# Optimization experiments

Measured on AMD Instinct MI355X. Metric: run time of the kernel, lower is better.

Reference implementation:

```python
import jax, jax.numpy as jnp
import numpy as np

B, C, L, H = 4, 512, 2048, 8
D = C // H  # head_dim


def setup_inputs() -> dict:
    key = jax.random.key(0)
    ks = jax.random.split(key, 9)
    s = 1.0 / np.sqrt(C)  # keep logits well-scaled like torch Linear init
    return {
        "x": jax.random.normal(ks[0], (B, C, L), dtype=jnp.float32),
        "Wq": jax.random.normal(ks[1], (C, C), dtype=jnp.float32) * s,
        "bq": jnp.zeros((C,), dtype=jnp.float32),
        "Wk": jax.random.normal(ks[2], (C, C), dtype=jnp.float32) * s,
        "bk": jnp.zeros((C,), dtype=jnp.float32),
        "Wv": jax.random.normal(ks[3], (C, C), dtype=jnp.float32) * s,
        "bv": jnp.zeros((C,), dtype=jnp.float32),
        "Wo": jax.random.normal(ks[4], (C, C), dtype=jnp.float32) * s,
        "bo": jnp.zeros((C,), dtype=jnp.float32),
    }


def reference(x, Wq, bq, Wk, bk, Wv, bv, Wo, bo):
    # x: (B, C, L) -> (B, L, C)
    xp = jnp.transpose(x, (0, 2, 1))
    scale = D ** (-0.5)

    def heads(w, b):
        y = xp @ w.T + b                      # (B, L, C)  torch Linear: x W^T + b
        return y.reshape(B, L, H, D).transpose(0, 2, 1, 3)  # (B, H, L, D)

    q = heads(Wq, bq)
    k = heads(Wk, bk)
    v = heads(Wv, bv)

    attn = jnp.einsum('bhqd,bhkd->bhqk', q, k) * scale  # (B, H, L, L)
    attn = jax.nn.softmax(attn, axis=-1)
    out = jnp.einsum('bhqk,bhkd->bhqd', attn, v)        # (B, H, L, D)
    out = out.transpose(0, 2, 1, 3).reshape(B, L, C)    # (B, L, C)
    out = out @ Wo.T + bo
    return x + jnp.transpose(out, (0, 2, 1))            # residual in (B, C, L)
```

## Files before the change

kernel.cpp:

```cpp
#include <hip/hip_runtime.h>
#include <math.h>

#define B_ 4
#define C_ 512
#define L_ 2048
#define H_ 8
#define D_ 64
#define QSCALE 0.18033688011112042f
#define DEFER_THR 12.0f

typedef __bf16 bf16x8 __attribute__((ext_vector_type(8)));
typedef float f32x4 __attribute__((ext_vector_type(4)));
typedef float f32x16 __attribute__((ext_vector_type(16)));

__device__ __forceinline__ unsigned cvt_pk(float lo, float hi) {
    unsigned r;
    asm("v_cvt_pk_bf16_f32 %0, %1, %2" : "=v"(r) : "v"(lo), "v"(hi));
    return r;
}
__device__ __forceinline__ unsigned short f2bf_hw(float a) {
    unsigned r;
    asm("v_cvt_pk_bf16_f32 %0, %1, %1" : "=v"(r) : "v"(a));
    return (unsigned short)r;
}
__device__ __forceinline__ bf16x8 frag_ld(const unsigned short* p) {
    uint4 v = *reinterpret_cast<const uint4*>(p);
    return __builtin_bit_cast(bf16x8, v);
}
__device__ __forceinline__ float fmax3(float a, float b, float c) {
    return fmaxf(fmaxf(a, b), c);
}
__device__ __forceinline__ void glds16(const void* g, void* l) {
    __builtin_amdgcn_global_load_lds(
        (const __attribute__((address_space(1))) void*)g,
        (__attribute__((address_space(3))) void*)l, 16, 0, 0);
}

__global__ __launch_bounds__(256) void prep(
    const float* __restrict__ x,
    const float* __restrict__ w0, const float* __restrict__ w1,
    const float* __restrict__ w2, const float* __restrict__ w3,
    unsigned short* __restrict__ xt,
    unsigned short* __restrict__ o0, unsigned short* __restrict__ o1,
    unsigned short* __restrict__ o2, unsigned short* __restrict__ o3)
{
    __shared__ float T[64][68];
    const int t = threadIdx.x;

    if (blockIdx.z < B_) {
        const int b  = blockIdx.z;
        const int l0 = blockIdx.x * 64;
        const int c0 = blockIdx.y * 64;
        const float* xb = x + (size_t)b * C_ * L_;
        unsigned short* xtb = xt + (size_t)b * L_ * C_;

        #pragma unroll
        for (int p = 0; p < 4; ++p) {
            const int ci = 16 * p + (t >> 4);
            const int l4 = (t & 15) * 4;
            *reinterpret_cast<float4*>(&T[ci][l4]) =
                *reinterpret_cast<const float4*>(xb + (size_t)(c0 + ci) * L_ + l0 + l4);
        }
        __syncthreads();

        const int lo = t >> 2;
        const int cb = (t & 3) * 16;
        unsigned w[8];
        #pragma unroll
        for (int k = 0; k < 8; ++k)
            w[k] = cvt_pk(T[cb + 2 * k][lo], T[cb + 2 * k + 1][lo]);
        unsigned short* dst = xtb + (size_t)(l0 + lo) * C_ + c0 + cb;
        *reinterpret_cast<uint4*>(dst)     = make_uint4(w[0], w[1], w[2], w[3]);
        *reinterpret_cast<uint4*>(dst + 8) = make_uint4(w[4], w[5], w[6], w[7]);
    } else {
        const int m = blockIdx.z - B_;
        const float* src; unsigned short* dst;
        if      (m == 0) { src = w0; dst = o0; }
        else if (m == 1) { src = w1; dst = o1; }
        else if (m == 2) { src = w2; dst = o2; }
        else             { src = w3; dst = o3; }
        const int flat = blockIdx.x + 32 * blockIdx.y;
        const size_t idx = ((size_t)flat * 256 + t) * 4;
        const float4 v = *reinterpret_cast<const float4*>(src + idx);
        *reinterpret_cast<uint2*>(dst + idx) =
            make_uint2(cvt_pk(v.x, v.y), cvt_pk(v.z, v.w));
    }
}

__global__ __launch_bounds__(256) void qkv_gemm(
    const unsigned short* __restrict__ xt,
    const unsigned short* __restrict__ wq, const unsigned short* __restrict__ wk,
    const unsigned short* __restrict__ wv,
    const float* __restrict__ bq, const float* __restrict__ bk,
    const float* __restrict__ bv,
    unsigned short* __restrict__ qb, unsigned short* __restrict__ kb,
    unsigned short* __restrict__ vb)
{
    __shared__ unsigned short As[2][128][32];
    __shared__ unsigned short Bs[2][128][32];

    const int mode = blockIdx.z >> 2;
    const int b    = blockIdx.z & 3;
    const size_t LC = (size_t)L_ * C_;

    const unsigned short *A, *Bt;
    const float* bias;
    unsigned short* Out;
    float scale = 1.0f;
    int m0, n0, oN, biasN;
    if (mode == 0) {
        A = xt + (size_t)b * LC; Bt = wq; bias = bq; Out = qb + (size_t)b * LC;
        m0 = blockIdx.y * 128; n0 = blockIdx.x * 128; oN = C_; biasN = 1;
        scale = QSCALE;
    } else if (mode == 1) {
        A = xt + (size_t)b * LC; Bt = wk; bias = bk; Out = kb + (size_t)b * LC;
        m0 = blockIdx.y * 128; n0 = blockIdx.x * 128; oN = C_; biasN = 1;
    } else {
        A = wv; Bt = xt + (size_t)b * LC; bias = bv; Out = vb + (size_t)b * LC;
        m0 = blockIdx.x * 128; n0 = blockIdx.y * 128; oN = L_; biasN = 0;
    }
    const int doswz = (mode != 0);

    const int t = threadIdx.x;
    const int lane = t & 63, wid = t >> 6;
    const int wm = (wid >> 1) * 64, wn = (wid & 1) * 64;
    const int q16 = lane & 15, g = lane >> 4;

    const int gr = wid * 32 + (lane >> 2);
    const int gc = (lane & 3) * 8;
    const unsigned short* Ap0 = A  + (size_t)(m0 + gr) * C_ + gc;
    const unsigned short* Ap1 = Ap0 + 16 * C_;
    const unsigned short* Bp0 = Bt + (size_t)(n0 + gr) * C_ + gc;
    const unsigned short* Bp1 = Bp0 + 16 * C_;

    f32x4 zero4 = {0.f, 0.f, 0.f, 0.f};
    f32x4 acc[4][4];
    #pragma unroll
    for (int i = 0; i < 4; ++i)
        #pragma unroll
        for (int j = 0; j < 4; ++j) acc[i][j] = zero4;

    glds16(Ap0, &As[0][wid * 32][0]);      glds16(Ap1, &As[0][wid * 32 + 16][0]);
    glds16(Bp0, &Bs[0][wid * 32][0]);      glds16(Bp1, &Bs[0][wid * 32 + 16][0]);
    __syncthreads();

    #pragma unroll 2
    for (int it = 0; it < 16; ++it) {
        const int cur = it & 1;
        if (it < 15) {
            const int ko = (it + 1) * 32;
            glds16(Ap0 + ko, &As[cur ^ 1][wid * 32][0]);
            glds16(Ap1 + ko, &As[cur ^ 1][wid * 32 + 16][0]);
            glds16(Bp0 + ko, &Bs[cur ^ 1][wid * 32][0]);
            glds16(Bp1 + ko, &Bs[cur ^ 1][wid * 32 + 16][0]);
        }
        bf16x8 af[4], bfr[4];
        #pragma unroll
        for (int i = 0; i < 4; ++i) af[i]  = frag_ld(&As[cur][wm + 16 * i + q16][8 * g]);
        #pragma unroll
        for (int j = 0; j < 4; ++j) bfr[j] = frag_ld(&Bs[cur][wn + 16 * j + q16][8 * g]);
        #pragma unroll
        for (int i = 0; i < 4; ++i)
            #pragma unroll
            for (int j = 0; j < 4; ++j)
                acc[i][j] = __builtin_amdgcn_mfma_f32_16x16x32_bf16(
                    af[i], bfr[j], acc[i][j], 0, 0, 0);
        __syncthreads();
    }

    #pragma unroll
    for (int j = 0; j < 4; ++j) {
        const int n = n0 + wn + 16 * j + q16;
        const float bn = biasN ? bias[n] : 0.f;
        #pragma unroll
        for (int i = 0; i < 4; ++i) {
            #pragma unroll
            for (int r = 0; r < 4; ++r) {
                const int m = m0 + wm + 16 * i + 4 * g + r;
                const float v = acc[i][j][r] + (biasN ? bn : bias[m]);
                const int nn = doswz ? (n ^ ((m & 7) << 3)) : n;
                Out[(size_t)m * oN + nn] = f2bf_hw(v * scale);
            }
        }
    }
}

__global__ __launch_bounds__(256) void gemm_out(
    const unsigned short* __restrict__ A,
    const unsigned short* __restrict__ Bt,
    const float* __restrict__ bias,
    float* __restrict__ Out, const float* __restrict__ resid)
{
    __shared__ unsigned short As[2][128][32];
    __shared__ unsigned short Bs[2][128][32];

    const int bz = blockIdx.z;
    const size_t LC = (size_t)L_ * C_;
    Bt    += (size_t)bz * LC;
    Out   += (size_t)bz * LC;
    resid += (size_t)bz * LC;

    const int n0 = blockIdx.x * 128;
    const int m0 = blockIdx.y * 128;
    const int t  = threadIdx.x;
    const int lane = t & 63, wid = t >> 6;
    const int wm = (wid >> 1) * 64, wn = (wid & 1) * 64;
    const int q16 = lane & 15, g = lane >> 4;

    const int gr = wid * 32 + (lane >> 2);
    const int gc = (lane & 3) * 8;
    const unsigned short* Ap0 = A  + (size_t)(m0 + gr) * C_ + gc;
    const unsigned short* Ap1 = Ap0 + 16 * C_;
    const unsigned short* Bp0 = Bt + (size_t)(n0 + gr) * C_ + gc;
    const unsigned short* Bp1 = Bp0 + 16 * C_;

    f32x4 zero4 = {0.f, 0.f, 0.f, 0.f};
    f32x4 acc[4][4];
    #pragma unroll
    for (int i = 0; i < 4; ++i)
        #pragma unroll
        for (int j = 0; j < 4; ++j) acc[i][j] = zero4;

    glds16(Ap0, &As[0][wid * 32][0]);      glds16(Ap1, &As[0][wid * 32 + 16][0]);
    glds16(Bp0, &Bs[0][wid * 32][0]);      glds16(Bp1, &Bs[0][wid * 32 + 16][0]);
    __syncthreads();

    #pragma unroll 2
    for (int it = 0; it < 16; ++it) {
        const int cur = it & 1;
        if (it < 15) {
            const int ko = (it + 1) * 32;
            glds16(Ap0 + ko, &As[cur ^ 1][wid * 32][0]);
            glds16(Ap1 + ko, &As[cur ^ 1][wid * 32 + 16][0]);
            glds16(Bp0 + ko, &Bs[cur ^ 1][wid * 32][0]);
            glds16(Bp1 + ko, &Bs[cur ^ 1][wid * 32 + 16][0]);
        }
        bf16x8 af[4], bfr[4];
        #pragma unroll
        for (int i = 0; i < 4; ++i) af[i]  = frag_ld(&As[cur][wm + 16 * i + q16][8 * g]);
        #pragma unroll
        for (int j = 0; j < 4; ++j) bfr[j] = frag_ld(&Bs[cur][wn + 16 * j + q16][8 * g]);
        #pragma unroll
        for (int i = 0; i < 4; ++i)
            #pragma unroll
            for (int j = 0; j < 4; ++j)
                acc[i][j] = __builtin_amdgcn_mfma_f32_16x16x32_bf16(
                    af[i], bfr[j], acc[i][j], 0, 0, 0);
        __syncthreads();
    }

    #pragma unroll
    for (int j = 0; j < 4; ++j) {
        const int n = n0 + wn + 16 * j + q16;
        #pragma unroll
        for (int i = 0; i < 4; ++i) {
            #pragma unroll
            for (int r = 0; r < 4; ++r) {
                const int m = m0 + wm + 16 * i + 4 * g + r;
                const size_t off = (size_t)m * L_ + n;
                Out[off] = acc[i][j][r] + bias[m] + resid[off];
            }
        }
    }
}

__global__ __launch_bounds__(256) void attn_mfma(
    const unsigned short* __restrict__ Qb,
    const unsigned short* __restrict__ Kb,
    const unsigned short* __restrict__ Vb,
    unsigned short* __restrict__ Ab)
{
    __shared__ unsigned short Ks[2][64][64];
    __shared__ unsigned short Vs[2][64][64];

    const int q0 = blockIdx.x * 128;
    const int h  = blockIdx.y;
    const int b  = blockIdx.z;
    const int t  = threadIdx.x, lane = t & 63, wid = t >> 6;
    const int q32 = lane & 31, hi = lane >> 5;
    const int swz = (q32 & 7) << 3;

    const unsigned short* Qg = Qb + (size_t)b * L_ * C_;
    const unsigned short* Kg = Kb + (size_t)b * L_ * C_ + h * D_;
    const unsigned short* Vg = Vb + ((size_t)b * C_ + h * D_) * L_;
    unsigned short* Ag       = Ab + (size_t)b * L_ * C_;

    bf16x8 qf[4];
    {
        const unsigned short* qp =
            Qg + (size_t)(q0 + 32 * wid + q32) * C_ + h * D_ + 8 * hi;
        #pragma unroll
        for (int c = 0; c < 4; ++c) qf[c] = frag_ld(qp + 16 * c);
    }

    const unsigned ow = (q32 == 0) ? 0x3F803F80u : 0u;
    const uint4 ov = make_uint4(ow, ow, ow, ow);
    const bf16x8 onesf = __builtin_bit_cast(bf16x8, ov);

    f32x16 zero16 = {0.f,0.f,0.f,0.f,0.f,0.f,0.f,0.f,
                     0.f,0.f,0.f,0.f,0.f,0.f,0.f,0.f};
    f32x16 oacc0 = zero16, oacc1 = zero16, lacc = zero16;
    float m_s = -INFINITY;

    const int gr8 = lane >> 3;
    const int gc8 = (lane & 7) * 8;
    const unsigned short* Kp0 = Kg + (size_t)(16 * wid + gr8) * C_ + gc8;
    const unsigned short* Kp1 = Kp0 + (size_t)8 * C_;
    const unsigned short* Vp0 = Vg + (size_t)(16 * wid + gr8) * L_ + gc8;
    const unsigned short* Vp1 = Vp0 + (size_t)8 * L_;

    glds16(Kp0, &Ks[0][16 * wid][0]);
    glds16(Kp1, &Ks[0][16 * wid + 8][0]);
    glds16(Vp0, &Vs[0][16 * wid][0]);
    glds16(Vp1, &Vs[0][16 * wid + 8][0]);
    __syncthreads();

    #pragma unroll 2
    for (int kt = 0; kt < 32; ++kt) {
        const int cur = kt & 1;
        if (kt < 31) {
            const size_t ko = (size_t)(kt + 1) * 64;
            glds16(Kp0 + ko * C_, &Ks[cur ^ 1][16 * wid][0]);
            glds16(Kp1 + ko * C_, &Ks[cur ^ 1][16 * wid + 8][0]);
            glds16(Vp0 + ko,      &Vs[cur ^ 1][16 * wid][0]);
            glds16(Vp1 + ko,      &Vs[cur ^ 1][16 * wid + 8][0]);
        }

        f32x16 s0 = zero16, s1 = zero16;
        #pragma unroll
        for (int c = 0; c < 4; ++c) {
            const int co = (16 * c + 8 * hi) ^ swz;
            bf16x8 k0 = frag_ld(&Ks[cur][q32][co]);
            bf16x8 k1 = frag_ld(&Ks[cur][32 + q32][co]);
            s0 = __builtin_amdgcn_mfma_f32_32x32x16_bf16(k0, qf[c], s0, 0, 0, 0);
            s1 = __builtin_amdgcn_mfma_f32_32x32x16_bf16(k1, qf[c], s1, 0, 0, 0);
        }

        const float a0 = fmax3(s0[0], s0[1], s0[2]);
        const float a1 = fmax3(s0[3], s0[4], s0[5]);
        const float a2 = fmax3(s0[6], s0[7], s0[8]);
        const float a3 = fmax3(s0[9], s0[10], s0[11]);
        const float a4 = fmax3(s0[12], s0[13], s0[14]);
        const float a5 = fmax3(s0[15], s1[0], s1[1]);
        const float a6 = fmax3(s1[2], s1[3], s1[4]);
        const float a7 = fmax3(s1[5], s1[6], s1[7]);
        const float a8 = fmax3(s1[8], s1[9], s1[10]);
        const float a9 = fmax3(s1[11], s1[12], s1[13]);
        const float b0 = fmax3(a0, a1, a2);
        const float b1 = fmax3(a3, a4, a5);
        const float b2 = fmax3(a6, a7, a8);
        const float b3 = fmax3(a9, s1[14], s1[15]);
        float pm = fmaxf(fmaxf(b0, b1), fmaxf(b2, b3));
        pm = fmaxf(pm, __shfl_xor(pm, 32));

        if (!__all(pm - m_s <= DEFER_THR)) {
            const float mn   = fmaxf(m_s, pm);
            const float corr = exp2f(m_s - mn);
            m_s = mn;
            #pragma unroll
            for (int r = 0; r < 16; ++r) {
                const float cr = __shfl(corr, (r & 3) + 8 * (r >> 2) + 4 * hi);
                oacc0[r] *= cr; oacc1[r] *= cr; lacc[r] *= cr;
            }
        }

        float p0[16], p1[16];
        #pragma unroll
        for (int r = 0; r < 16; ++r) {
            p0[r] = exp2f(s0[r] - m_s);
            p1[r] = exp2f(s1[r] - m_s);
        }

        #pragma unroll
        for (int ks = 0; ks < 4; ++ks) {
            const int rb = 8 * (ks & 1);
            #define PPX(i) ((ks < 2) ? p0[(i)] : p1[(i)])
            unsigned wa = cvt_pk(PPX(rb + 0), PPX(rb + 1));
            unsigned wb = cvt_pk(PPX(rb + 2), PPX(rb + 3));
            unsigned wc = cvt_pk(PPX(rb + 4), PPX(rb + 5));
            unsigned wd = cvt_pk(PPX(rb + 6), PPX(rb + 7));
            #undef PPX
            asm volatile("v_permlane32_swap_b32 %0, %1" : "+v"(wa), "+v"(wc));
            asm volatile("v_permlane32_swap_b32 %0, %1" : "+v"(wb), "+v"(wd));
            const uint4 pv = make_uint4(wa, wb, wc, wd);
            const bf16x8 paf = __builtin_bit_cast(bf16x8, pv);

            const int co = (16 * ks + 8 * hi) ^ swz;
            bf16x8 v0 = frag_ld(&Vs[cur][q32][co]);
            bf16x8 v1 = frag_ld(&Vs[cur][32 + q32][co]);
            oacc0 = __builtin_amdgcn_mfma_f32_32x32x16_bf16(paf, v0, oacc0, 0, 0, 0);
            oacc1 = __builtin_amdgcn_mfma_f32_32x32x16_bf16(paf, v1, oacc1, 0, 0, 0);
            lacc  = __builtin_amdgcn_mfma_f32_32x32x16_bf16(paf, onesf, lacc, 0, 0, 0);
        }

        __syncthreads();
    }

    #pragma unroll
    for (int r = 0; r < 16; ++r) {
        const float lv  = __shfl(lacc[r], hi << 5);
        const float inv = 1.f / lv;
        const int q = q0 + 32 * wid + (r & 3) + 8 * (r >> 2) + 4 * hi;
        unsigned short* op = Ag + (size_t)q * C_ + h * D_ + q32;
        op[0]  = f2bf_hw(oacc0[r] * inv);
        op[32] = f2bf_hw(oacc1[r] * inv);
    }
}

extern "C" void kernel_launch(void* const* d_in, const int* in_sizes, int n_in,
                              void* d_out, int out_size, void* d_ws, size_t ws_size,
                              hipStream_t stream)
{
    const float* x  = (const float*)d_in[0];
    const float* Wq = (const float*)d_in[1];
    const float* bq = (const float*)d_in[2];
    const float* Wk = (const float*)d_in[3];
    const float* bk = (const float*)d_in[4];
    const float* Wv = (const float*)d_in[5];
    const float* bv = (const float*)d_in[6];
    const float* Wo = (const float*)d_in[7];
    const float* bo = (const float*)d_in[8];
    float* out = (float*)d_out;

    const size_t NB = (size_t)B_ * L_ * C_;
    const size_t NW = (size_t)C_ * C_;
    unsigned short* ws16 = (unsigned short*)d_ws;
    unsigned short* xt  = ws16;
    unsigned short* qb  = xt  + NB;
    unsigned short* kb  = qb  + NB;
    unsigned short* vb  = kb  + NB;
    unsigned short* att = vb  + NB;
    unsigned short* wqb = att + NB;
    unsigned short* wkb = wqb + NW;
    unsigned short* wvb = wkb + NW;
    unsigned short* wob = wvb + NW;

    prep<<<dim3(32, 8, 2 * B_), 256, 0, stream>>>(
        x, Wq, Wk, Wv, Wo, xt, wqb, wkb, wvb, wob);

    qkv_gemm<<<dim3(4, 16, 3 * B_), 256, 0, stream>>>(
        xt, wqb, wkb, wvb, bq, bk, bv, qb, kb, vb);

    attn_mfma<<<dim3(L_ / 128, H_, B_), 256, 0, stream>>>(qb, kb, vb, att);

    gemm_out<<<dim3(16, 4, B_), 256, 0, stream>>>(wob, att, bo, out, x);
}
```

Measured before the change: 208.6 us.

## Split attention KV range in two halves and merge partials; single-buffer GEMMs

The attention kernel now splits the key/value sequence into two halves across the grid, doubling the block count from 512 to 1024 to improve occupancy on the many-CU device. Each half writes unnormalized fp32 partial outputs plus running max and sum, and a new merge kernel combines them with log-sum-exp weights into bf16. The QKV and output GEMMs also drop LDS double buffering: one uses synchronous single-buffer direct loads, the other register-prefetch into a padded LDS tile. The cost is an extra kernel launch, extra fp32 partial traffic, and possibly less load/compute overlap in the GEMMs.

```diff
diff --git a/kernel.cpp b/kernel.cpp
--- a/kernel.cpp
+++ b/kernel.cpp
@@ -96,8 +96,8 @@
     unsigned short* __restrict__ qb, unsigned short* __restrict__ kb,
     unsigned short* __restrict__ vb)
 {
-    __shared__ unsigned short As[2][128][32];
-    __shared__ unsigned short Bs[2][128][32];
+    __shared__ unsigned short As[128][32];
+    __shared__ unsigned short Bs[128][32];
 
     const int mode = blockIdx.z >> 2;
     const int b    = blockIdx.z & 3;
@@ -132,6 +132,10 @@
     const unsigned short* Ap1 = Ap0 + 16 * C_;
     const unsigned short* Bp0 = Bt + (size_t)(n0 + gr) * C_ + gc;
     const unsigned short* Bp1 = Bp0 + 16 * C_;
+    unsigned short* lA0 = &As[wid * 32][0];
+    unsigned short* lA1 = &As[wid * 32 + 16][0];
+    unsigned short* lB0 = &Bs[wid * 32][0];
+    unsigned short* lB1 = &Bs[wid * 32 + 16][0];
 
     f32x4 zero4 = {0.f, 0.f, 0.f, 0.f};
     f32x4 acc[4][4];
@@ -140,32 +144,22 @@
         #pragma unroll
         for (int j = 0; j < 4; ++j) acc[i][j] = zero4;
 
-    glds16(Ap0, &As[0][wid * 32][0]);      glds16(Ap1, &As[0][wid * 32 + 16][0]);
-    glds16(Bp0, &Bs[0][wid * 32][0]);      glds16(Bp1, &Bs[0][wid * 32 + 16][0]);
-    __syncthreads();
-
-    #pragma unroll 2
-    for (int it = 0; it < 16; ++it) {
-        const int cur = it & 1;
-        if (it < 15) {
-            const int ko = (it + 1) * 32;
-            glds16(Ap0 + ko, &As[cur ^ 1][wid * 32][0]);
-            glds16(Ap1 + ko, &As[cur ^ 1][wid * 32 + 16][0]);
-            glds16(Bp0 + ko, &Bs[cur ^ 1][wid * 32][0]);
-            glds16(Bp1 + ko, &Bs[cur ^ 1][wid * 32 + 16][0]);
-        }
+    for (int k0 = 0; k0 < C_; k0 += 32) {
+        __syncthreads();
+        glds16(Ap0 + k0, lA0); glds16(Ap1 + k0, lA1);
+        glds16(Bp0 + k0, lB0); glds16(Bp1 + k0, lB1);
+        __syncthreads();
         bf16x8 af[4], bfr[4];
         #pragma unroll
-        for (int i = 0; i < 4; ++i) af[i]  = frag_ld(&As[cur][wm + 16 * i + q16][8 * g]);
-        #pragma unroll
-        for (int j = 0; j < 4; ++j) bfr[j] = frag_ld(&Bs[cur][wn + 16 * j + q16][8 * g]);
+        for (int i = 0; i < 4; ++i) af[i]  = frag_ld(&As[wm + 16 * i + q16][8 * g]);
+        #pragma unroll
+        for (int j = 0; j < 4; ++j) bfr[j] = frag_ld(&Bs[wn + 16 * j + q16][8 * g]);
         #pragma unroll
         for (int i = 0; i < 4; ++i)
             #pragma unroll
             for (int j = 0; j < 4; ++j)
                 acc[i][j] = __builtin_amdgcn_mfma_f32_16x16x32_bf16(
                     af[i], bfr[j], acc[i][j], 0, 0, 0);
-        __syncthreads();
     }
 
     #pragma unroll
@@ -191,8 +185,8 @@
     const float* __restrict__ bias,
     float* __restrict__ Out, const float* __restrict__ resid)
 {
-    __shared__ unsigned short As[2][128][32];
-    __shared__ unsigned short Bs[2][128][32];
+    __shared__ unsigned short As[128][40];
+    __shared__ unsigned short Bs[128][40];
 
     const int bz = blockIdx.z;
     const size_t LC = (size_t)L_ * C_;
@@ -207,12 +201,10 @@
     const int wm = (wid >> 1) * 64, wn = (wid & 1) * 64;
     const int q16 = lane & 15, g = lane >> 4;
 
-    const int gr = wid * 32 + (lane >> 2);
-    const int gc = (lane & 3) * 8;
-    const unsigned short* Ap0 = A  + (size_t)(m0 + gr) * C_ + gc;
-    const unsigned short* Ap1 = Ap0 + 16 * C_;
-    const unsigned short* Bp0 = Bt + (size_t)(n0 + gr) * C_ + gc;
-    const unsigned short* Bp1 = Bp0 + 16 * C_;
+    const int srow = t >> 1;
+    const int scol = (t & 1) * 16;
+    const unsigned short* Ap = A  + (size_t)(m0 + srow) * C_ + scol;
+    const unsigned short* Bp = Bt + (size_t)(n0 + srow) * C_ + scol;
 
     f32x4 zero4 = {0.f, 0.f, 0.f, 0.f};
     f32x4 acc[4][4];
@@ -221,32 +213,35 @@
         #pragma unroll
         for (int j = 0; j < 4; ++j) acc[i][j] = zero4;
 
-    glds16(Ap0, &As[0][wid * 32][0]);      glds16(Ap1, &As[0][wid * 32 + 16][0]);
-    glds16(Bp0, &Bs[0][wid * 32][0]);      glds16(Bp1, &Bs[0][wid * 32 + 16][0]);
-    __syncthreads();
-
-    #pragma unroll 2
-    for (int it = 0; it < 16; ++it) {
-        const int cur = it & 1;
-        if (it < 15) {
-            const int ko = (it + 1) * 32;
-            glds16(Ap0 + ko, &As[cur ^ 1][wid * 32][0]);
-            glds16(Ap1 + ko, &As[cur ^ 1][wid * 32 + 16][0]);
-            glds16(Bp0 + ko, &Bs[cur ^ 1][wid * 32][0]);
-            glds16(Bp1 + ko, &Bs[cur ^ 1][wid * 32 + 16][0]);
+    uint4 ar0 = *reinterpret_cast<const uint4*>(Ap);
+    uint4 ar1 = *reinterpret_cast<const uint4*>(Ap + 8);
+    uint4 br0 = *reinterpret_cast<const uint4*>(Bp);
+    uint4 br1 = *reinterpret_cast<const uint4*>(Bp + 8);
+
+    for (int k0 = 0; k0 < C_; k0 += 32) {
+        __syncthreads();
+        *reinterpret_cast<uint4*>(&As[srow][scol])     = ar0;
+        *reinterpret_cast<uint4*>(&As[srow][scol + 8]) = ar1;
+        *reinterpret_cast<uint4*>(&Bs[srow][scol])     = br0;
+        *reinterpret_cast<uint4*>(&Bs[srow][scol + 8]) = br1;
+        __syncthreads();
+        if (k0 + 32 < C_) {
+            ar0 = *reinterpret_cast<const uint4*>(Ap + k0 + 32);
+            ar1 = *reinterpret_cast<const uint4*>(Ap + k0 + 40);
+            br0 = *reinterpret_cast<const uint4*>(Bp + k0 + 32);
+            br1 = *reinterpret_cast<const uint4*>(Bp + k0 + 40);
         }
         bf16x8 af[4], bfr[4];
         #pragma unroll
-        for (int i = 0; i < 4; ++i) af[i]  = frag_ld(&As[cur][wm + 16 * i + q16][8 * g]);
-        #pragma unroll
-        for (int j = 0; j < 4; ++j) bfr[j] = frag_ld(&Bs[cur][wn + 16 * j + q16][8 * g]);
+        for (int i = 0; i < 4; ++i) af[i]  = frag_ld(&As[wm + 16 * i + q16][8 * g]);
+        #pragma unroll
+        for (int j = 0; j < 4; ++j) bfr[j] = frag_ld(&Bs[wn + 16 * j + q16][8 * g]);
         #pragma unroll
         for (int i = 0; i < 4; ++i)
             #pragma unroll
             for (int j = 0; j < 4; ++j)
                 acc[i][j] = __builtin_amdgcn_mfma_f32_16x16x32_bf16(
                     af[i], bfr[j], acc[i][j], 0, 0, 0);
-        __syncthreads();
     }
 
     #pragma unroll
@@ -268,22 +263,24 @@
     const unsigned short* __restrict__ Qb,
     const unsigned short* __restrict__ Kb,
     const unsigned short* __restrict__ Vb,
-    unsigned short* __restrict__ Ab)
+    float* __restrict__ opart, float2* __restrict__ mlb)
 {
     __shared__ unsigned short Ks[2][64][64];
     __shared__ unsigned short Vs[2][64][64];
 
-    const int q0 = blockIdx.x * 128;
-    const int h  = blockIdx.y;
-    const int b  = blockIdx.z;
+    const int q0   = blockIdx.x * 128;
+    const int h    = blockIdx.y;
+    const int b    = blockIdx.z >> 1;
+    const int half = blockIdx.z & 1;
     const int t  = threadIdx.x, lane = t & 63, wid = t >> 6;
     const int q32 = lane & 31, hi = lane >> 5;
     const int swz = (q32 & 7) << 3;
 
     const unsigned short* Qg = Qb + (size_t)b * L_ * C_;
-    const unsigned short* Kg = Kb + (size_t)b * L_ * C_ + h * D_;
-    const unsigned short* Vg = Vb + ((size_t)b * C_ + h * D_) * L_;
-    unsigned short* Ag       = Ab + (size_t)b * L_ * C_;
+    const unsigned short* Kg = Kb + (size_t)b * L_ * C_ + h * D_
+                                  + (size_t)half * (L_ / 2) * C_;
+    const unsigned short* Vg = Vb + ((size_t)b * C_ + h * D_) * L_
+                                  + (size_t)half * (L_ / 2);
 
     bf16x8 qf[4];
     {
@@ -316,9 +313,9 @@
     __syncthreads();
 
     #pragma unroll 2
-    for (int kt = 0; kt < 32; ++kt) {
+    for (int kt = 0; kt < 16; ++kt) {
         const int cur = kt & 1;
-        if (kt < 31) {
+        if (kt < 15) {
             const size_t ko = (size_t)(kt + 1) * 64;
             glds16(Kp0 + ko * C_, &Ks[cur ^ 1][16 * wid][0]);
             glds16(Kp1 + ko * C_, &Ks[cur ^ 1][16 * wid + 8][0]);
@@ -396,15 +393,61 @@
         __syncthreads();
     }
 
+    const size_t PST = (size_t)B_ * H_ * L_ * D_;
+    float* op = opart + (size_t)half * PST + ((size_t)b * H_ + h) * L_ * D_;
+    float2* mlp = mlb + (size_t)half * (B_ * H_ * L_) + ((size_t)b * H_ + h) * L_;
+
     #pragma unroll
     for (int r = 0; r < 16; ++r) {
-        const float lv  = __shfl(lacc[r], hi << 5);
-        const float inv = 1.f / lv;
-        const int q = q0 + 32 * wid + (r & 3) + 8 * (r >> 2) + 4 * hi;
-        unsigned short* op = Ag + (size_t)q * C_ + h * D_ + q32;
-        op[0]  = f2bf_hw(oacc0[r] * inv);
-        op[32] = f2bf_hw(oacc1[r] * inv);
-    }
+        const int crow = (r & 3) + 8 * (r >> 2) + 4 * hi;
+        const int q = q0 + 32 * wid + crow;
+        const float lv = __shfl(lacc[r], hi << 5);
+        const float mo = __shfl(m_s, crow);
+        float* o = op + (size_t)q * D_ + q32;
+        o[0]  = oacc0[r];
+        o[32] = oacc1[r];
+        if (q32 == 0) mlp[q] = make_float2(mo, lv);
+    }
+}
+
+__global__ __launch_bounds__(256) void merge_halves(
+    const float* __restrict__ opart, const float2* __restrict__ mlb,
+    unsigned short* __restrict__ att)
+{
+    const size_t PST = (size_t)B_ * H_ * L_ * D_;
+    const int idx = blockIdx.x * 256 + threadIdx.x;
+    const int d8 = idx & 7;
+    const int l  = (idx >> 3) & (L_ - 1);
+    const int bh = idx >> 14;
+    const int b  = bh >> 3, h = bh & 7;
+
+    const size_t base = ((size_t)bh * L_ + l) * D_ + d8 * 8;
+    const float4 x0 = *reinterpret_cast<const float4*>(opart + base);
+    const float4 x1 = *reinterpret_cast<const float4*>(opart + base + 4);
+    const float4 y0 = *reinterpret_cast<const float4*>(opart + PST + base);
+    const float4 y1 = *reinterpret_cast<const float4*>(opart + PST + base + 4);
+
+    const float2 ml0 = mlb[(size_t)bh * L_ + l];
+    const float2 ml1 = mlb[(size_t)B_ * H_ * L_ + (size_t)bh * L_ + l];
+
+    const float ms = fmaxf(ml0.x, ml1.x);
+    const float w0 = exp2f(ml0.x - ms);
+    const float w1 = exp2f(ml1.x - ms);
+    const float inv = 1.0f / (ml0.y * w0 + ml1.y * w1);
+    const float wa = w0 * inv, wb = w1 * inv;
+
+    const float r0 = x0.x * wa + y0.x * wb;
+    const float r1 = x0.y * wa + y0.y * wb;
+    const float r2 = x0.z * wa + y0.z * wb;
+    const float r3 = x0.w * wa + y0.w * wb;
+    const float r4 = x1.x * wa + y1.x * wb;
+    const float r5 = x1.y * wa + y1.y * wb;
+    const float r6 = x1.z * wa + y1.z * wb;
+    const float r7 = x1.w * wa + y1.w * wb;
+
+    unsigned short* dst = att + (size_t)b * L_ * C_ + (size_t)l * C_ + h * D_ + d8 * 8;
+    *reinterpret_cast<uint4*>(dst) = make_uint4(
+        cvt_pk(r0, r1), cvt_pk(r2, r3), cvt_pk(r4, r5), cvt_pk(r6, r7));
 }
 
 extern "C" void kernel_launch(void* const* d_in, const int* in_sizes, int n_in,
@@ -434,6 +477,8 @@
     unsigned short* wkb = wqb + NW;
     unsigned short* wvb = wkb + NW;
     unsigned short* wob = wvb + NW;
+    float* opart = (float*)(wob + NW);
+    float2* mlb  = (float2*)(opart + 2 * (size_t)B_ * H_ * L_ * D_);
 
     prep<<<dim3(32, 8, 2 * B_), 256, 0, stream>>>(
         x, Wq, Wk, Wv, Wo, xt, wqb, wkb, wvb, wob);
@@ -441,7 +486,11 @@
     qkv_gemm<<<dim3(4, 16, 3 * B_), 256, 0, stream>>>(
         xt, wqb, wkb, wvb, bq, bk, bv, qb, kb, vb);
 
-    attn_mfma<<<dim3(L_ / 128, H_, B_), 256, 0, stream>>>(qb, kb, vb, att);
+    attn_mfma<<<dim3(L_ / 128, H_, 2 * B_), 256, 0, stream>>>(
+        qb, kb, vb, opart, mlb);
+
+    merge_halves<<<dim3(B_ * H_ * L_ * 8 / 256), 256, 0, stream>>>(
+        opart, mlb, att);
 
     gemm_out<<<dim3(16, 4, B_), 256, 0, stream>>>(wob, att, bo, out, x);
 }
```

Result: faster. 200.1 us (-4.1%).
